# Performance work log

Measured on AMD Instinct MI355X. Metric: run time of the kernel, lower is better.

## Reference

```python
import jax, jax.numpy as jnp
import numpy as np

B, T, D = 2, 1024, 384
d = D // 3            # 128
D3 = 3 * d            # 384
D9 = 9 * d            # 1152
GAMMA = 5.0
EPS_W = 1e-8
EPS_N = 1e-5


def _orth(rng, n):
    q, _ = np.linalg.qr(rng.standard_normal((n, n)).astype(np.float64))
    return jnp.asarray(q.astype(np.float32))


def setup_inputs() -> dict:
    key = jax.random.key(0)
    x = jax.random.normal(key, (B, T, D), dtype=jnp.float32)
    rng = np.random.default_rng(0)
    def plin(fan_in, fan_out):
        W = jnp.asarray(rng.standard_normal((fan_out, fan_in)).astype(np.float32) * 0.05)
        b = jnp.zeros((fan_out,), jnp.float32)
        return W, b
    Wq, bq = plin(d, D3); Sq = _orth(rng, D3)
    Wk, bk = plin(d, D3); Sk = _orth(rng, D3)
    Wv, bv = plin(d, D3); Sv = _orth(rng, D3)
    Wp, bp = plin(D3, D9)
    gn = jnp.ones((D9,), jnp.float32)
    bn = jnp.zeros((D9,), jnp.float32)
    return {"x": x, "Wq": Wq, "bq": bq, "Sq": Sq, "Wk": Wk, "bk": bk, "Sk": Sk,
            "Wv": Wv, "bv": bv, "Sv": Sv, "Wp": Wp, "bp": bp, "gn": gn, "bn": bn}


def _plin(x, W, b):
    # PositiveLinearHK: linear with softplus-positive weights
    return x @ jax.nn.softplus(W).T + b


def reference(x, Wq, bq, Sq, Wk, bk, Sk, Wv, bv, Sv, Wp, bp, gn, bn):
    Q_base = x[:, :, 0 * d:1 * d]
    K_base = x[:, :, 1 * d:2 * d]
    V_base = x[:, :, 2 * d:3 * d]
    # proj = PositiveLinearHK -> SingleStiefelProjector (orthogonal mixing)
    Q = _plin(Q_base, Wq, bq) @ Sq          # (B,T,3d)
    K = _plin(K_base, Wk, bk) @ Sk
    V = _plin(V_base, Wv, bv) @ Sv
    dots = jnp.einsum('bti,btj->btij', Q, K)            # (B,T,3d,3d)
    scores = jax.nn.sigmoid(GAMMA * dots)
    weights = scores / (scores.sum(axis=-1, keepdims=True) + EPS_W)
    attended = jnp.einsum('btij,btj->bti', weights, V)  # (B,T,3d)
    h = _plin(attended, Wp, bp)                         # (B,T,9d)
    mu = h.mean(axis=-1, keepdims=True)
    var = h.var(axis=-1, keepdims=True)
    return (h - mu) * jax.lax.rsqrt(var + EPS_N) * gn + bn
```

## Files before the change

### kernel.cpp

```cpp
#include <hip/hip_runtime.h>
#include <hip/hip_bf16.h>
#include <math.h>

#define NTOK  2048
#define DD    128
#define DD3   384
#define DD9   1152
#define TB    2
#define TBQ   4
#define TBP   4
#define GAMMA_F 5.0f
#define LN2_F   0.69314718f
#define LOG2E_F 1.44269504f

#define OFF_M    0
#define OFF_C    147456
#define OFF_BP   148608
#define OFF_ATT  369792
#define OFF_SSUM 763008
#define OFF_QKV  765056

typedef __attribute__((ext_vector_type(8))) short bf16x8;
typedef __attribute__((ext_vector_type(4))) float f32x4;

__device__ __forceinline__ float softplusf(float x) {
    return fmaxf(x, 0.0f) + log1pf(__expf(-fabsf(x)));
}
__device__ __forceinline__ unsigned short f2bf(float f) {
    __hip_bfloat16 h = __float2bfloat16(f);
    return *reinterpret_cast<unsigned short*>(&h);
}
__device__ __forceinline__ float bf2f(unsigned short u) {
    return __uint_as_float(((unsigned)u) << 16);
}
__device__ __forceinline__ float exp2_fast(float x) {
#if __has_builtin(__builtin_amdgcn_exp2f)
    return __builtin_amdgcn_exp2f(x);
#else
    return __expf(x * LN2_F);
#endif
}

__global__ __launch_bounds__(384) void k_prep(const float* __restrict__ Wq, const float* __restrict__ Wk,
                                              const float* __restrict__ Wv, const float* __restrict__ Wp,
                                              const float* __restrict__ Sq, const float* __restrict__ Sk,
                                              const float* __restrict__ Sv, const float* __restrict__ bq,
                                              const float* __restrict__ bk, const float* __restrict__ bv,
                                              float* __restrict__ ws) {
    __shared__ float sw[DD3];
    int b = blockIdx.x, tid = threadIdx.x;
    if (b < 576) {
        int idx = b * 384 + tid;
        unsigned lo = f2bf(softplusf(Wp[2 * idx + 0]) - LN2_F);
        unsigned hi = f2bf(softplusf(Wp[2 * idx + 1]) - LN2_F);
        ((unsigned*)(ws + OFF_BP))[idx] = lo | (hi << 16);
    } else if (b < 960) {
        int bb = b - 576;
        int mat = bb >> 7, i = bb & 127;
        const float* W = (mat == 0) ? Wq : (mat == 1 ? Wk : Wv);
        const float* S = (mat == 0) ? Sq : (mat == 1 ? Sk : Sv);
        int m = tid;
        sw[m] = softplusf(W[m * DD + i]);
        __syncthreads();
        const float4* sw4 = (const float4*)sw;
        float a0 = 0.f, a1 = 0.f, a2 = 0.f, a3 = 0.f;
        for (int j4 = 0; j4 < 96; ++j4) {
            float4 w = sw4[j4];
            int j = j4 * 4;
            a0 = fmaf(w.x, S[(j + 0) * DD3 + m], a0);
            a1 = fmaf(w.y, S[(j + 1) * DD3 + m], a1);
            a2 = fmaf(w.z, S[(j + 2) * DD3 + m], a2);
            a3 = fmaf(w.w, S[(j + 3) * DD3 + m], a3);
        }
        ws[OFF_M + mat * 49152 + (i >> 2) * (DD3 * 4) + m * 4 + (i & 3)] = (a0 + a1) + (a2 + a3);
    } else {
        int mat = b - 960;
        const float* S = (mat == 0) ? Sq : (mat == 1 ? Sk : Sv);
        const float* bb_ = (mat == 0) ? bq : (mat == 1 ? bk : bv);
        int m = tid;
        float a0 = 0.f, a1 = 0.f, a2 = 0.f, a3 = 0.f;
        for (int j4 = 0; j4 < 96; ++j4) {
            int j = j4 * 4;
            a0 = fmaf(bb_[j + 0], S[(j + 0) * DD3 + m], a0);
            a1 = fmaf(bb_[j + 1], S[(j + 1) * DD3 + m], a1);
            a2 = fmaf(bb_[j + 2], S[(j + 2) * DD3 + m], a2);
            a3 = fmaf(bb_[j + 3], S[(j + 3) * DD3 + m], a3);
        }
        ws[OFF_C + mat * DD3 + m] = (a0 + a1) + (a2 + a3);
    }
}

__global__ __launch_bounds__(384, 3) void k_qkv(const float* __restrict__ x,
                                                float* __restrict__ ws) {
    int tid = threadIdx.x;
    int tok0 = blockIdx.x * TBQ;
    const float* xb = x + (size_t)tok0 * DD3;
    float* qg = ws + OFF_QKV + (size_t)tok0 * DD9;
#pragma unroll
    for (int mat = 0; mat < 3; ++mat) {
        const float4* M4 = (const float4*)(ws + OFF_M + mat * 49152);
        const float* xt0 = xb + 0 * DD3 + mat * DD;
        const float* xt1 = xb + 1 * DD3 + mat * DD;
        const float* xt2 = xb + 2 * DD3 + mat * DD;
        const float* xt3 = xb + 3 * DD3 + mat * DD;
        float a0 = 0.f, a1 = 0.f, a2 = 0.f, a3 = 0.f;
        for (int i4 = 0; i4 < 32; ++i4) {
            float4 mm = M4[i4 * DD3 + tid];
            int i = i4 * 4;
            a0 = fmaf(xt0[i], mm.x, fmaf(xt0[i + 1], mm.y, fmaf(xt0[i + 2], mm.z, fmaf(xt0[i + 3], mm.w, a0))));
            a1 = fmaf(xt1[i], mm.x, fmaf(xt1[i + 1], mm.y, fmaf(xt1[i + 2], mm.z, fmaf(xt1[i + 3], mm.w, a1))));
            a2 = fmaf(xt2[i], mm.x, fmaf(xt2[i + 1], mm.y, fmaf(xt2[i + 2], mm.z, fmaf(xt2[i + 3], mm.w, a2))));
            a3 = fmaf(xt3[i], mm.x, fmaf(xt3[i + 1], mm.y, fmaf(xt3[i + 2], mm.z, fmaf(xt3[i + 3], mm.w, a3))));
        }
        float c = ws[OFF_C + mat * DD3 + tid];
        qg[0 * DD9 + mat * DD3 + tid] = a0 + c;
        qg[1 * DD9 + mat * DD3 + tid] = a1 + c;
        qg[2 * DD9 + mat * DD3 + tid] = a2 + c;
        qg[3 * DD9 + mat * DD3 + tid] = a3 + c;
    }
}

#define SIGROW(NQ, RS, AV) do {                                        \
        float e0 = exp2_fast((NQ) * kk.x);                             \
        float e1 = exp2_fast((NQ) * kk.y);                             \
        float e2 = exp2_fast((NQ) * kk.z);                             \
        float e3 = exp2_fast((NQ) * kk.w);                             \
        float s0 = __builtin_amdgcn_rcpf(1.0f + e0);                   \
        float s1 = __builtin_amdgcn_rcpf(1.0f + e1);                   \
        float s2 = __builtin_amdgcn_rcpf(1.0f + e2);                   \
        float s3 = __builtin_amdgcn_rcpf(1.0f + e3);                   \
        RS += (s0 + s1) + (s2 + s3);                                   \
        AV = fmaf(s0, vv.x, fmaf(s1, vv.y, fmaf(s2, vv.z, fmaf(s3, vv.w, AV)))); \
    } while (0)

__global__ __launch_bounds__(384, 6) void k_sig(float* __restrict__ ws) {
    __shared__ float att[TB * DD3];
    __shared__ float red[16];
    int tid = threadIdx.x;
    int tok0 = blockIdx.x * TB;
    int t  = __builtin_amdgcn_readfirstlane(tid / 192);
    int ts = tid - t * 192;
    const float* qkvg = ws + OFF_QKV + (size_t)(tok0 + t) * DD9;

    float nq0 = qkvg[ts]       * (-GAMMA_F * LOG2E_F);
    float nq1 = qkvg[ts + 192] * (-GAMMA_F * LOG2E_F);
    const float4* K4 = (const float4*)(qkvg + DD3);
    const float4* V4 = (const float4*)(qkvg + 2 * DD3);
    float rs0 = 0.f, rs1 = 0.f, av0 = 0.f, av1 = 0.f;
    for (int j4 = 0; j4 < 96; ++j4) {
        float4 kk = K4[j4];
        float4 vv = V4[j4];
        SIGROW(nq0, rs0, av0);
        SIGROW(nq1, rs1, av1);
    }
    float a0 = av0 * __builtin_amdgcn_rcpf(rs0 + 1e-8f);
    float a1 = av1 * __builtin_amdgcn_rcpf(rs1 + 1e-8f);
    unsigned short b0 = f2bf(a0), b1 = f2bf(a1);
    att[t * DD3 + ts]       = bf2f(b0);
    att[t * DD3 + ts + 192] = bf2f(b1);
    unsigned short* ag = (unsigned short*)(ws + OFF_ATT);
    ag[(size_t)(tok0 + t) * DD3 + ts]       = b0;
    ag[(size_t)(tok0 + t) * DD3 + ts + 192] = b1;
    __syncthreads();

    int wave = tid >> 6, lane64 = tid & 63;
    float s0 = att[0 * DD3 + tid];
    float s1 = att[1 * DD3 + tid];
#pragma unroll
    for (int off = 32; off; off >>= 1) {
        s0 += __shfl_down(s0, off, 64);
        s1 += __shfl_down(s1, off, 64);
    }
    if (lane64 == 0) { red[wave] = s0; red[8 + wave] = s1; }
    __syncthreads();
    if (tid < TB) {
        float a = 0.f;
        for (int w = 0; w < 6; ++w) a += red[tid * 8 + w];
        ws[OFF_SSUM + tok0 + tid] = a;
    }
}

__global__ __launch_bounds__(384, 3) void k_proj(const float* __restrict__ bp,
                                                 const float* __restrict__ gn,
                                                 const float* __restrict__ bn,
                                                 const float* __restrict__ ws,
                                                 float* __restrict__ out) {
    __shared__ unsigned short attb[16 * 392];
    __shared__ float h[TBP * DD9];
    __shared__ float red[32];
    __shared__ float smu[TBP], sinv[TBP];

    int tid = threadIdx.x;
    int wave = tid >> 6, lane64 = tid & 63;
    int tok0 = blockIdx.x * TBP;
    {
        const unsigned short* ag = (const unsigned short*)(ws + OFF_ATT) + (size_t)tok0 * DD3;
        if (tid < 192) {
            int r = tid / 48, c = (tid - r * 48) * 8;
            *(uint4*)(attb + r * 392 + c) = *(const uint4*)(ag + tid * 8);
        }
        unsigned* az = (unsigned*)(attb + 4 * 392);
        for (int idx = tid; idx < 2352; idx += 384) az[idx] = 0u;
    }
    __syncthreads();
    {
        int n0w  = wave * 192;
        int brow = lane64 & 15;
        int koff = (lane64 >> 4) * 8;
        const unsigned short* Bp = (const unsigned short*)(ws + OFF_BP);
        const unsigned short* abase = attb + brow * 392 + koff;
        const unsigned short* bbase = Bp + (size_t)(n0w + brow) * DD3 + koff;
        f32x4 acc[12];
#pragma unroll
        for (int nt = 0; nt < 12; ++nt) acc[nt] = (f32x4){0.f, 0.f, 0.f, 0.f};
        for (int ks = 0; ks < 12; ++ks) {
            bf16x8 a = *(const bf16x8*)(abase + ks * 32);
            const unsigned short* bk_ = bbase + ks * 32;
#pragma unroll
            for (int nt = 0; nt < 12; ++nt) {
                bf16x8 bfr = *(const bf16x8*)(bk_ + nt * 16 * DD3);
                acc[nt] = __builtin_amdgcn_mfma_f32_16x16x32_bf16(a, bfr, acc[nt], 0, 0, 0);
            }
        }
        if (lane64 < 16) {
            int col0 = n0w + lane64;
#pragma unroll
            for (int nt = 0; nt < 12; ++nt) {
#pragma unroll
                for (int r = 0; r < TBP; ++r)
                    h[r * DD9 + col0 + nt * 16] = acc[nt][r];
            }
        }
    }
    __syncthreads();

    const float* ssums = ws + OFF_SSUM + tok0;
    float acc3[3][TBP];
    {
        float bp0 = bp[tid], bp1 = bp[tid + DD3], bp2 = bp[tid + 2 * DD3];
#pragma unroll
        for (int t = 0; t < TBP; ++t) {
            float base = LN2_F * ssums[t];
            acc3[0][t] = h[t * DD9 + tid]           + bp0 + base;
            acc3[1][t] = h[t * DD9 + tid + DD3]     + bp1 + base;
            acc3[2][t] = h[t * DD9 + tid + 2 * DD3] + bp2 + base;
        }
    }
#pragma unroll
    for (int t = 0; t < TBP; ++t) {
        float s = acc3[0][t] + acc3[1][t] + acc3[2][t];
#pragma unroll
        for (int off = 32; off; off >>= 1) s += __shfl_down(s, off, 64);
        if (lane64 == 0) red[t * 8 + wave] = s;
    }
    __syncthreads();
    if (tid < TBP) {
        float a = 0.f;
        for (int w = 0; w < 6; ++w) a += red[tid * 8 + w];
        smu[tid] = a * (1.0f / 1152.0f);
    }
    __syncthreads();
#pragma unroll
    for (int t = 0; t < TBP; ++t) {
        float mu = smu[t];
        acc3[0][t] -= mu; acc3[1][t] -= mu; acc3[2][t] -= mu;
        float s = fmaf(acc3[0][t], acc3[0][t], fmaf(acc3[1][t], acc3[1][t], acc3[2][t] * acc3[2][t]));
#pragma unroll
        for (int off = 32; off; off >>= 1) s += __shfl_down(s, off, 64);
        if (lane64 == 0) red[t * 8 + wave] = s;
    }
    __syncthreads();
    if (tid < TBP) {
        float b = 0.f;
        for (int w = 0; w < 6; ++w) b += red[tid * 8 + w];
        sinv[tid] = __builtin_amdgcn_rsqf(b * (1.0f / 1152.0f) + 1e-5f);
    }
    __syncthreads();
    float g0 = gn[tid], g1 = gn[tid + DD3], g2 = gn[tid + 2 * DD3];
    float b0 = bn[tid], b1 = bn[tid + DD3], b2 = bn[tid + 2 * DD3];
#pragma unroll
    for (int t = 0; t < TBP; ++t) {
        float inv = sinv[t];
        size_t base = (size_t)(tok0 + t) * DD9;
        out[base + tid]           = fmaf(acc3[0][t] * inv, g0, b0);
        out[base + tid + DD3]     = fmaf(acc3[1][t] * inv, g1, b1);
        out[base + tid + 2 * DD3] = fmaf(acc3[2][t] * inv, g2, b2);
    }
}

extern "C" void kernel_launch(void* const* d_in, const int* in_sizes, int n_in,
                              void* d_out, int out_size, void* d_ws, size_t ws_size,
                              hipStream_t stream) {
    const float* x  = (const float*)d_in[0];
    const float* Wq = (const float*)d_in[1];
    const float* bq = (const float*)d_in[2];
    const float* Sq = (const float*)d_in[3];
    const float* Wk = (const float*)d_in[4];
    const float* bk = (const float*)d_in[5];
    const float* Sk = (const float*)d_in[6];
    const float* Wv = (const float*)d_in[7];
    const float* bv = (const float*)d_in[8];
    const float* Sv = (const float*)d_in[9];
    const float* Wp = (const float*)d_in[10];
    const float* bp = (const float*)d_in[11];
    const float* gn = (const float*)d_in[12];
    const float* bn = (const float*)d_in[13];
    float* out = (float*)d_out;
    float* ws  = (float*)d_ws;

    hipLaunchKernelGGL(k_prep, dim3(963), dim3(384), 0, stream,
                       Wq, Wk, Wv, Wp, Sq, Sk, Sv, bq, bk, bv, ws);
    hipLaunchKernelGGL(k_qkv, dim3(NTOK / TBQ), dim3(384), 0, stream, x, ws);
    hipLaunchKernelGGL(k_sig, dim3(NTOK / TB), dim3(384), 0, stream, ws);
    hipLaunchKernelGGL(k_proj, dim3(NTOK / TBP), dim3(384), 0, stream, bp, gn, bn, ws, out);
}
```

Baseline: 160.7 us.

## Move attended-row sum into projection kernel and widen projection token tile

The sigmoid kernel now writes only the bf16 attended vector and drops its shared-memory staging, block reduction and per-token sum output. The projection kernel recomputes each token's row sum from the bf16 attended values and reads MFMA A-fragments straight from global memory rather than a zero-padded LDS tile. Its token tile grows from 4 to 8 so all 16 MFMA rows carry two copies of the 8 tokens instead of 12 padding rows. The QKV kernel is halved to 2 tokens per block with higher occupancy. This cuts barriers and launch-side work at the cost of more direct global loads and more LDS for h.

```diff
diff --git a/kernel.cpp b/kernel.cpp
--- a/kernel.cpp
+++ b/kernel.cpp
@@ -7,8 +7,8 @@
 #define DD3   384
 #define DD9   1152
 #define TB    2
-#define TBQ   4
-#define TBP   4
+#define TBQ   2
+#define TBP   8
 #define GAMMA_F 5.0f
 #define LN2_F   0.69314718f
 #define LOG2E_F 1.44269504f
@@ -17,7 +17,6 @@
 #define OFF_C    147456
 #define OFF_BP   148608
 #define OFF_ATT  369792
-#define OFF_SSUM 763008
 #define OFF_QKV  765056
 
 typedef __attribute__((ext_vector_type(8))) short bf16x8;
@@ -90,7 +89,7 @@
     }
 }
 
-__global__ __launch_bounds__(384, 3) void k_qkv(const float* __restrict__ x,
+__global__ __launch_bounds__(384, 6) void k_qkv(const float* __restrict__ x,
                                                 float* __restrict__ ws) {
     int tid = threadIdx.x;
     int tok0 = blockIdx.x * TBQ;
@@ -101,22 +100,16 @@
         const float4* M4 = (const float4*)(ws + OFF_M + mat * 49152);
         const float* xt0 = xb + 0 * DD3 + mat * DD;
         const float* xt1 = xb + 1 * DD3 + mat * DD;
-        const float* xt2 = xb + 2 * DD3 + mat * DD;
-        const float* xt3 = xb + 3 * DD3 + mat * DD;
-        float a0 = 0.f, a1 = 0.f, a2 = 0.f, a3 = 0.f;
+        float a0 = 0.f, a1 = 0.f;
         for (int i4 = 0; i4 < 32; ++i4) {
             float4 mm = M4[i4 * DD3 + tid];
             int i = i4 * 4;
             a0 = fmaf(xt0[i], mm.x, fmaf(xt0[i + 1], mm.y, fmaf(xt0[i + 2], mm.z, fmaf(xt0[i + 3], mm.w, a0))));
             a1 = fmaf(xt1[i], mm.x, fmaf(xt1[i + 1], mm.y, fmaf(xt1[i + 2], mm.z, fmaf(xt1[i + 3], mm.w, a1))));
-            a2 = fmaf(xt2[i], mm.x, fmaf(xt2[i + 1], mm.y, fmaf(xt2[i + 2], mm.z, fmaf(xt2[i + 3], mm.w, a2))));
-            a3 = fmaf(xt3[i], mm.x, fmaf(xt3[i + 1], mm.y, fmaf(xt3[i + 2], mm.z, fmaf(xt3[i + 3], mm.w, a3))));
         }
         float c = ws[OFF_C + mat * DD3 + tid];
         qg[0 * DD9 + mat * DD3 + tid] = a0 + c;
         qg[1 * DD9 + mat * DD3 + tid] = a1 + c;
-        qg[2 * DD9 + mat * DD3 + tid] = a2 + c;
-        qg[3 * DD9 + mat * DD3 + tid] = a3 + c;
     }
 }
 
@@ -134,8 +127,6 @@
     } while (0)
 
 __global__ __launch_bounds__(384, 6) void k_sig(float* __restrict__ ws) {
-    __shared__ float att[TB * DD3];
-    __shared__ float red[16];
     int tid = threadIdx.x;
     int tok0 = blockIdx.x * TB;
     int t  = __builtin_amdgcn_readfirstlane(tid / 192);
@@ -155,60 +146,45 @@
     }
     float a0 = av0 * __builtin_amdgcn_rcpf(rs0 + 1e-8f);
     float a1 = av1 * __builtin_amdgcn_rcpf(rs1 + 1e-8f);
-    unsigned short b0 = f2bf(a0), b1 = f2bf(a1);
-    att[t * DD3 + ts]       = bf2f(b0);
-    att[t * DD3 + ts + 192] = bf2f(b1);
     unsigned short* ag = (unsigned short*)(ws + OFF_ATT);
-    ag[(size_t)(tok0 + t) * DD3 + ts]       = b0;
-    ag[(size_t)(tok0 + t) * DD3 + ts + 192] = b1;
-    __syncthreads();
-
-    int wave = tid >> 6, lane64 = tid & 63;
-    float s0 = att[0 * DD3 + tid];
-    float s1 = att[1 * DD3 + tid];
-#pragma unroll
-    for (int off = 32; off; off >>= 1) {
-        s0 += __shfl_down(s0, off, 64);
-        s1 += __shfl_down(s1, off, 64);
-    }
-    if (lane64 == 0) { red[wave] = s0; red[8 + wave] = s1; }
-    __syncthreads();
-    if (tid < TB) {
-        float a = 0.f;
-        for (int w = 0; w < 6; ++w) a += red[tid * 8 + w];
-        ws[OFF_SSUM + tok0 + tid] = a;
-    }
-}
-
-__global__ __launch_bounds__(384, 3) void k_proj(const float* __restrict__ bp,
-                                                 const float* __restrict__ gn,
-                                                 const float* __restrict__ bn,
-                                                 const float* __restrict__ ws,
-                                                 float* __restrict__ out) {
-    __shared__ unsigned short attb[16 * 392];
+    ag[(size_t)(tok0 + t) * DD3 + ts]       = f2bf(a0);
+    ag[(size_t)(tok0 + t) * DD3 + ts + 192] = f2bf(a1);
+}
+
+__global__ __launch_bounds__(384) void k_proj(const float* __restrict__ bp,
+                                              const float* __restrict__ gn,
+                                              const float* __restrict__ bn,
+                                              const float* __restrict__ ws,
+                                              float* __restrict__ out) {
     __shared__ float h[TBP * DD9];
-    __shared__ float red[32];
-    __shared__ float smu[TBP], sinv[TBP];
+    __shared__ float red[64];
+    __shared__ float ssum[TBP], smu[TBP], sinv[TBP];
 
     int tid = threadIdx.x;
     int wave = tid >> 6, lane64 = tid & 63;
     int tok0 = blockIdx.x * TBP;
-    {
-        const unsigned short* ag = (const unsigned short*)(ws + OFF_ATT) + (size_t)tok0 * DD3;
-        if (tid < 192) {
-            int r = tid / 48, c = (tid - r * 48) * 8;
-            *(uint4*)(attb + r * 392 + c) = *(const uint4*)(ag + tid * 8);
-        }
-        unsigned* az = (unsigned*)(attb + 4 * 392);
-        for (int idx = tid; idx < 2352; idx += 384) az[idx] = 0u;
-    }
-    __syncthreads();
+    const unsigned short* ag = (const unsigned short*)(ws + OFF_ATT);
+
+#pragma unroll
+    for (int r = 0; r < TBP; ++r) {
+        float s = bf2f(ag[(size_t)(tok0 + r) * DD3 + tid]);
+#pragma unroll
+        for (int off = 32; off; off >>= 1) s += __shfl_down(s, off, 64);
+        if (lane64 == 0) red[r * 8 + wave] = s;
+    }
+    __syncthreads();
+    if (tid < TBP) {
+        float a = 0.f;
+        for (int w = 0; w < 6; ++w) a += red[tid * 8 + w];
+        ssum[tid] = a;
+    }
+
     {
         int n0w  = wave * 192;
         int brow = lane64 & 15;
         int koff = (lane64 >> 4) * 8;
         const unsigned short* Bp = (const unsigned short*)(ws + OFF_BP);
-        const unsigned short* abase = attb + brow * 392 + koff;
+        const unsigned short* abase = ag + (size_t)(tok0 + (brow & 7)) * DD3 + koff;
         const unsigned short* bbase = Bp + (size_t)(n0w + brow) * DD3 + koff;
         f32x4 acc[12];
 #pragma unroll
@@ -222,25 +198,25 @@
                 acc[nt] = __builtin_amdgcn_mfma_f32_16x16x32_bf16(a, bfr, acc[nt], 0, 0, 0);
             }
         }
-        if (lane64 < 16) {
-            int col0 = n0w + lane64;
+        if (lane64 < 32) {
+            int rbase = (lane64 >> 4) * 4;
+            int col0  = n0w + (lane64 & 15);
 #pragma unroll
             for (int nt = 0; nt < 12; ++nt) {
 #pragma unroll
-                for (int r = 0; r < TBP; ++r)
-                    h[r * DD9 + col0 + nt * 16] = acc[nt][r];
+                for (int r = 0; r < 4; ++r)
+                    h[(rbase + r) * DD9 + col0 + nt * 16] = acc[nt][r];
             }
         }
     }
     __syncthreads();
 
-    const float* ssums = ws + OFF_SSUM + tok0;
     float acc3[3][TBP];
     {
         float bp0 = bp[tid], bp1 = bp[tid + DD3], bp2 = bp[tid + 2 * DD3];
 #pragma unroll
         for (int t = 0; t < TBP; ++t) {
-            float base = LN2_F * ssums[t];
+            float base = LN2_F * ssum[t];
             acc3[0][t] = h[t * DD9 + tid]           + bp0 + base;
             acc3[1][t] = h[t * DD9 + tid + DD3]     + bp1 + base;
             acc3[2][t] = h[t * DD9 + tid + 2 * DD3] + bp2 + base;
```

Measured after the change: 151.0 us. 6.1% less time.
